# Kernel optimization log

Hardware: AMD Instinct MI355X
Metric: run time of the kernel (lower is better)

## Reference

```python
import jax, jax.numpy as jnp
import numpy as np

B, N_IN, N_OUT = 16, 7000, 28000
C_IN, C_OUT, S = 64, 64, 9
NNZ = 3 * N_OUT  # ~3 source verts per upsampled vert (barycentric)


def setup_inputs() -> dict:
    key = jax.random.key(0)
    k = jax.random.split(key, 6)
    x = jax.random.normal(k[0], (B, N_IN, C_IN), dtype=jnp.float32)
    values = jax.random.uniform(k[1], (NNZ,), dtype=jnp.float32)
    row = jax.random.randint(k[2], (NNZ,), 0, N_OUT)
    col = jax.random.randint(k[3], (NNZ,), 0, N_IN)
    spiral_indices = jax.random.randint(k[4], (N_OUT, S), 0, N_OUT)
    weight = jax.random.normal(k[5], (S * C_IN, C_OUT), dtype=jnp.float32) * 0.02
    bias = jnp.zeros((C_OUT,), dtype=jnp.float32)
    return {"x": x, "values": values, "weight": weight, "bias": bias,
            "row": row, "col": col, "spiral_indices": spiral_indices}


def reference(x, values, weight, bias, row, col, spiral_indices):
    # Pool: gather source verts, scale by sparse matrix values, scatter-add to output verts
    n_out = spiral_indices.shape[0]
    gathered = x[:, col, :] * values[None, :, None]            # [B, nnz, C]
    pooled = jnp.zeros((x.shape[0], n_out, x.shape[2]), x.dtype).at[:, row, :].add(gathered)  # [B, N_out, C]
    # SpiralConv: gather spiral neighborhood, flatten, linear
    feat = pooled[:, spiral_indices.reshape(-1), :]            # [B, N_out*S, C]
    feat = feat.reshape(x.shape[0], n_out, -1)                 # [B, N_out, S*C]
    out = jax.nn.elu(jnp.einsum('bnf,fo->bno', feat, weight) + bias)
    return out
```

## Files before the change

### kernel.cpp

```cpp
#include <hip/hip_runtime.h>
#include <math.h>

#define B      16
#define N_IN   7000
#define N_OUT  28000
#define C      64
#define S      9
#define NNZ    (3 * N_OUT)
#define F      (S * C)
#define KB     (F / 32)

typedef short bf16x8 __attribute__((ext_vector_type(8)));
typedef float f32x4  __attribute__((ext_vector_type(4)));

static __device__ __forceinline__ unsigned short f2bf(float f) {
    unsigned u = __float_as_uint(f);
    u += 0x7fffu + ((u >> 16) & 1u);
    return (unsigned short)(u >> 16);
}

__global__ void hist_kernel(const int* __restrict__ row, int* __restrict__ cnt) {
    int i = blockIdx.x * 256 + threadIdx.x;
    if (i < NNZ) atomicAdd(&cnt[row[i]], 1);
}

__global__ void scan_kernel(const int* __restrict__ cnt,
                            int* __restrict__ offs, int* __restrict__ cursor) {
    __shared__ int tmp[1024];
    const int t = threadIdx.x;
    const int base = t * 28;
    const bool live = (t < 1000);

    int c[28];
    int partial = 0;
    if (live) {
        #pragma unroll
        for (int j = 0; j < 28; ++j) { c[j] = cnt[base + j]; partial += c[j]; }
    }
    tmp[t] = partial;
    __syncthreads();
    #pragma unroll
    for (int off = 1; off < 1024; off <<= 1) {
        int v = (t >= off) ? tmp[t - off] : 0;
        __syncthreads();
        tmp[t] += v;
        __syncthreads();
    }
    if (live) {
        int run = tmp[t] - partial;
        #pragma unroll
        for (int j = 0; j < 28; ++j) {
            offs[base + j]   = run;
            cursor[base + j] = run;
            run += c[j];
        }
        if (t == 999) offs[N_OUT] = run;
    }
}

__global__ void place_kernel(const int* __restrict__ row, const int* __restrict__ col,
                             const float* __restrict__ values,
                             int* __restrict__ cursor,
                             int* __restrict__ ecol, float* __restrict__ eval) {
    int i = blockIdx.x * 256 + threadIdx.x;
    if (i < NNZ) {
        int pos = atomicAdd(&cursor[row[i]], 1);
        ecol[pos] = col[i];
        eval[pos] = values[i];
    }
}

__global__ void xt_kernel(const float* __restrict__ x, float* __restrict__ xT) {
    const int n  = blockIdx.x;
    const int t  = threadIdx.x;
    const int b  = t >> 4;
    const int ch = (t & 15) * 4;
    const float4 v = *(const float4*)(x + ((size_t)b * N_IN + n) * C + ch);
    *(float4*)(xT + ((size_t)n * B + b) * C + ch) = v;
}

__global__ void pool_kernel(const float* __restrict__ xT,
                            const int*   __restrict__ ecol,
                            const float* __restrict__ eval,
                            const int*   __restrict__ offs,
                            unsigned short* __restrict__ pooled) {
    const int wave = threadIdx.x >> 6;
    const int lane = threadIdx.x & 63;
    const int r    = blockIdx.x * 4 + wave;

    const int start = offs[r], end = offs[r + 1];

    float4 acc[4];
    #pragma unroll
    for (int j = 0; j < 4; ++j) acc[j] = make_float4(0.f, 0.f, 0.f, 0.f);

    for (int e = start; e < end; ++e) {
        const int   cl = ecol[e];
        const float v  = eval[e];
        const float* base = xT + (size_t)cl * (B * C) + lane * 4;
        float4 xv[4];
        #pragma unroll
        for (int j = 0; j < 4; ++j)
            xv[j] = *(const float4*)(base + j * 256);
        #pragma unroll
        for (int j = 0; j < 4; ++j) {
            acc[j].x = fmaf(xv[j].x, v, acc[j].x);
            acc[j].y = fmaf(xv[j].y, v, acc[j].y);
            acc[j].z = fmaf(xv[j].z, v, acc[j].z);
            acc[j].w = fmaf(xv[j].w, v, acc[j].w);
        }
    }

    #pragma unroll
    for (int j = 0; j < 4; ++j) {
        const int g  = j >> 1;
        const int bp = (j & 1) * 4 + (lane >> 4);
        unsigned long long ov =
            (unsigned long long)f2bf(acc[j].x)
            | ((unsigned long long)f2bf(acc[j].y) << 16)
            | ((unsigned long long)f2bf(acc[j].z) << 32)
            | ((unsigned long long)f2bf(acc[j].w) << 48);
        unsigned short* dst = pooled + (size_t)g * (N_OUT * 512)
                            + (size_t)r * 512 + bp * 64 + (lane & 15) * 4;
        __builtin_nontemporal_store(ov, (unsigned long long*)dst);
    }
}

__global__ void packw_kernel(const float* __restrict__ w, unsigned short* __restrict__ pw) {
    const int kb   = blockIdx.x;
    const int nt   = threadIdx.x >> 6;
    const int lane = threadIdx.x & 63;
    const int lm   = lane & 15;
    const int quad = lane >> 4;

    unsigned short v[8];
    #pragma unroll
    for (int j = 0; j < 8; ++j) {
        const int k = kb * 32 + quad * 8 + j;
        const int n = nt * 16 + lm;
        v[j] = f2bf(w[(size_t)k * C + n]);
    }
    unsigned short* dst = pw + ((size_t)(kb * 4 + nt) * 64 + lane) * 8;
    #pragma unroll
    for (int j = 0; j < 8; ++j) dst[j] = v[j];
}

__global__ __launch_bounds__(512, 2)
void spiral_mfma(const unsigned short* __restrict__ pooled,
                 const bf16x8*         __restrict__ packedW,
                 const int*            __restrict__ sp,
                 const float*          __restrict__ bias,
                 float*                __restrict__ out) {
    const int Lb    = blockIdx.x;
    const int g     = Lb & 1;
    const int mtile = Lb >> 1;
    const int wave  = threadIdx.x >> 6;
    const int lane  = threadIdx.x & 63;
    const int lm    = lane & 15;
    const int quad  = lane >> 4;
    const int m_base = mtile * 32;
    const int b      = g * 8 + wave;

    __shared__ bf16x8         bw[KB * 4 * 64];
    __shared__ unsigned short apool[2][32][512];

    {
        const int t = threadIdx.x;
        #pragma unroll
        for (int i = 0; i < 9; ++i)
            bw[i * 512 + t] = packedW[i * 512 + t];
    }

    int spv[S];
    {
        const int r = m_base + (lane & 31);
        #pragma unroll
        for (int s = 0; s < S; ++s) spv[s] = sp[r * S + s];
    }

    const unsigned short* pgbase = pooled + (size_t)g * (N_OUT * 512);

    f32x4 acc[2][4];
    #pragma unroll
    for (int t = 0; t < 2; ++t)
        #pragma unroll
        for (int nt = 0; nt < 4; ++nt)
            acc[t][nt] = (f32x4){0.f, 0.f, 0.f, 0.f};

    bf16x8 ld[4];

    #pragma unroll
    for (int q = 0; q < 4; ++q) {
        const int r = __shfl(spv[0], wave * 4 + q, 64);
        ld[q] = *(const bf16x8*)(pgbase + (size_t)r * 512 + lane * 8);
    }
    #pragma unroll
    for (int q = 0; q < 4; ++q) {
        const int j = wave * 4 + q;
        *(bf16x8*)(&apool[0][j][(lane ^ (j & 7)) * 8]) = ld[q];
    }
    __syncthreads();

    #pragma unroll
    for (int s = 0; s < S; ++s) {
        const int cur = s & 1, nxt = cur ^ 1;

        if (s + 1 < S) {
            #pragma unroll
            for (int q = 0; q < 4; ++q) {
                const int r = __shfl(spv[s + 1], wave * 4 + q, 64);
                ld[q] = *(const bf16x8*)(pgbase + (size_t)r * 512 + lane * 8);
            }
        }

        #pragma unroll
        for (int half = 0; half < 2; ++half) {
            bf16x8 bb[4];
            #pragma unroll
            for (int nt = 0; nt < 4; ++nt)
                bb[nt] = bw[((s * 2 + half) * 4 + nt) * 64 + lane];
            bf16x8 aa[2];
            #pragma unroll
            for (int t = 0; t < 2; ++t) {
                const int j = t * 16 + lm;
                const int chunk = wave * 8 + (((half * 4 + quad) ^ (j & 7)));
                aa[t] = *(const bf16x8*)(&apool[cur][j][chunk * 8]);
            }
            #pragma unroll
            for (int nt = 0; nt < 4; ++nt)
                #pragma unroll
                for (int t = 0; t < 2; ++t)
                    acc[t][nt] = __builtin_amdgcn_mfma_f32_16x16x32_bf16(
                        aa[t], bb[nt], acc[t][nt], 0, 0, 0);
        }

        if (s + 1 < S) {
            #pragma unroll
            for (int q = 0; q < 4; ++q) {
                const int j = wave * 4 + q;
                *(bf16x8*)(&apool[nxt][j][(lane ^ (j & 7)) * 8]) = ld[q];
            }
        }
        __syncthreads();
    }

    #pragma unroll
    for (int nt = 0; nt < 4; ++nt) {
        const int n = nt * 16 + lm;
        const float bs = bias[n];
        #pragma unroll
        for (int t = 0; t < 2; ++t) {
            #pragma unroll
            for (int reg = 0; reg < 4; ++reg) {
                const int r = m_base + t * 16 + quad * 4 + reg;
                float v = acc[t][nt][reg] + bs;
                v = v > 0.f ? v : (__expf(v) - 1.0f);
                __builtin_nontemporal_store(v,
                    out + ((size_t)b * N_OUT + r) * C + n);
            }
        }
    }
}

extern "C" void kernel_launch(void* const* d_in, const int* in_sizes, int n_in,
                              void* d_out, int out_size, void* d_ws, size_t ws_size,
                              hipStream_t stream) {
    const float* x      = (const float*)d_in[0];
    const float* values = (const float*)d_in[1];
    const float* weight = (const float*)d_in[2];
    const float* bias   = (const float*)d_in[3];
    const int*   row    = (const int*)d_in[4];
    const int*   col    = (const int*)d_in[5];
    const int*   sp     = (const int*)d_in[6];
    float*       out    = (float*)d_out;

    char* ws = (char*)d_ws;
    size_t off = 0;
    unsigned short* pooled  = (unsigned short*)(ws + off); off += (size_t)B * N_OUT * C * 2;
    unsigned short* packedW = (unsigned short*)(ws + off); off += (size_t)KB * 4 * 64 * 8 * 2;
    float* xT     = (float*)(ws + off); off += (size_t)N_IN * B * C * 4;
    int*   offs   = (int*)(ws + off); off += ((size_t)(N_OUT + 1) * 4 + 124) / 128 * 128;
    int*   cursor = (int*)(ws + off); off += (size_t)N_OUT * 4 + 128;
    int*   cnt    = (int*)(ws + off); off += (size_t)N_OUT * 4 + 128;
    int*   ecol   = (int*)(ws + off); off += (size_t)NNZ * 4;
    float* eval   = (float*)(ws + off); off += (size_t)NNZ * 4;

    (void)hipMemsetAsync(cnt, 0, (size_t)N_OUT * 4, stream);
    hist_kernel <<<(NNZ + 255) / 256, 256, 0, stream>>>(row, cnt);
    scan_kernel <<<1, 1024, 0, stream>>>(cnt, offs, cursor);
    place_kernel<<<(NNZ + 255) / 256, 256, 0, stream>>>(row, col, values, cursor, ecol, eval);

    packw_kernel<<<KB, 256, 0, stream>>>(weight, packedW);

    xt_kernel<<<N_IN, 256, 0, stream>>>(x, xT);

    pool_kernel<<<N_OUT / 4, 256, 0, stream>>>(xT, ecol, eval, offs, pooled);

    spiral_mfma<<<875 * 2, 512, 0, stream>>>(pooled,
        reinterpret_cast<const bf16x8*>(packedW), sp, bias, out);
}
```

Measured before the change: 321.0 us.

## Drop x transpose kernel and gather directly from x with batch-split pool blocks

```diff
diff --git a/kernel.cpp b/kernel.cpp
--- a/kernel.cpp
+++ b/kernel.cpp
@@ -70,60 +70,57 @@
     }
 }
 
-__global__ void xt_kernel(const float* __restrict__ x, float* __restrict__ xT) {
-    const int n  = blockIdx.x;
-    const int t  = threadIdx.x;
-    const int b  = t >> 4;
-    const int ch = (t & 15) * 4;
-    const float4 v = *(const float4*)(x + ((size_t)b * N_IN + n) * C + ch);
-    *(float4*)(xT + ((size_t)n * B + b) * C + ch) = v;
-}
-
-__global__ void pool_kernel(const float* __restrict__ xT,
+__global__ void pool_kernel(const float* __restrict__ x,
                             const int*   __restrict__ ecol,
                             const float* __restrict__ eval,
                             const int*   __restrict__ offs,
                             unsigned short* __restrict__ pooled) {
+    const int bg     = blockIdx.x & 7;
+    const int rowblk = blockIdx.x >> 3;
     const int wave = threadIdx.x >> 6;
     const int lane = threadIdx.x & 63;
-    const int r    = blockIdx.x * 4 + wave;
+    const int rsub = lane >> 5;
+    const int bsub = (lane >> 4) & 1;
+    const int sl   = lane & 15;
+
+    const int r = rowblk * 8 + wave * 2 + rsub;
+    const int b = bg + 8 * bsub;
 
     const int start = offs[r], end = offs[r + 1];
 
-    float4 acc[4];
-    #pragma unroll
-    for (int j = 0; j < 4; ++j) acc[j] = make_float4(0.f, 0.f, 0.f, 0.f);
-
-    for (int e = start; e < end; ++e) {
-        const int   cl = ecol[e];
-        const float v  = eval[e];
-        const float* base = xT + (size_t)cl * (B * C) + lane * 4;
+    float4 acc = make_float4(0.f, 0.f, 0.f, 0.f);
+    const float* xb = x + (size_t)b * N_IN * C + sl * 4;
+
+    for (int e = start; e < end; e += 4) {
+        const int nn = end - e;
+        int   cl[4]; float vv[4];
+        #pragma unroll
+        for (int j = 0; j < 4; ++j) {
+            const int ee = (j < nn) ? e + j : e;
+            cl[j] = ecol[ee];
+            vv[j] = (j < nn) ? eval[ee] : 0.f;
+        }
         float4 xv[4];
         #pragma unroll
         for (int j = 0; j < 4; ++j)
-            xv[j] = *(const float4*)(base + j * 256);
+            xv[j] = *(const float4*)(xb + (size_t)cl[j] * C);
         #pragma unroll
         for (int j = 0; j < 4; ++j) {
-            acc[j].x = fmaf(xv[j].x, v, acc[j].x);
-            acc[j].y = fmaf(xv[j].y, v, acc[j].y);
-            acc[j].z = fmaf(xv[j].z, v, acc[j].z);
-            acc[j].w = fmaf(xv[j].w, v, acc[j].w);
-        }
-    }
-
-    #pragma unroll
-    for (int j = 0; j < 4; ++j) {
-        const int g  = j >> 1;
-        const int bp = (j & 1) * 4 + (lane >> 4);
-        unsigned long long ov =
-            (unsigned long long)f2bf(acc[j].x)
-            | ((unsigned long long)f2bf(acc[j].y) << 16)
-            | ((unsigned long long)f2bf(acc[j].z) << 32)
-            | ((unsigned long long)f2bf(acc[j].w) << 48);
-        unsigned short* dst = pooled + (size_t)g * (N_OUT * 512)
-                            + (size_t)r * 512 + bp * 64 + (lane & 15) * 4;
-        __builtin_nontemporal_store(ov, (unsigned long long*)dst);
-    }
+            acc.x = fmaf(xv[j].x, vv[j], acc.x);
+            acc.y = fmaf(xv[j].y, vv[j], acc.y);
+            acc.z = fmaf(xv[j].z, vv[j], acc.z);
+            acc.w = fmaf(xv[j].w, vv[j], acc.w);
+        }
+    }
+
+    unsigned long long ov =
+        (unsigned long long)f2bf(acc.x)
+        | ((unsigned long long)f2bf(acc.y) << 16)
+        | ((unsigned long long)f2bf(acc.z) << 32)
+        | ((unsigned long long)f2bf(acc.w) << 48);
+    unsigned short* dst = pooled + (size_t)bsub * (N_OUT * 512)
+                        + (size_t)r * 512 + bg * 64 + sl * 4;
+    __builtin_nontemporal_store(ov, (unsigned long long*)dst);
 }
 
 __global__ void packw_kernel(const float* __restrict__ w, unsigned short* __restrict__ pw) {
@@ -278,7 +275,6 @@
     size_t off = 0;
     unsigned short* pooled  = (unsigned short*)(ws + off); off += (size_t)B * N_OUT * C * 2;
     unsigned short* packedW = (unsigned short*)(ws + off); off += (size_t)KB * 4 * 64 * 8 * 2;
-    float* xT     = (float*)(ws + off); off += (size_t)N_IN * B * C * 4;
     int*   offs   = (int*)(ws + off); off += ((size_t)(N_OUT + 1) * 4 + 124) / 128 * 128;
     int*   cursor = (int*)(ws + off); off += (size_t)N_OUT * 4 + 128;
     int*   cnt    = (int*)(ws + off); off += (size_t)N_OUT * 4 + 128;
@@ -292,9 +288,7 @@
 
     packw_kernel<<<KB, 256, 0, stream>>>(weight, packedW);
 
-    xt_kernel<<<N_IN, 256, 0, stream>>>(x, xT);
-
-    pool_kernel<<<N_OUT / 4, 256, 0, stream>>>(xT, ecol, eval, offs, pooled);
+    pool_kernel<<<3500 * 8, 256, 0, stream>>>(x, ecol, eval, offs, pooled);
 
     spiral_mfma<<<875 * 2, 512, 0, stream>>>(pooled,
         reinterpret_cast<const bf16x8*>(packedW), sp, bias, out);
```

Measured after the change: 300.3 us. -6.4%, faster.
